# Kernel tuning notes

Measured on AMD Instinct MI355X. Metric: run time of the kernel, lower is better.

## Reference

```python
import jax, jax.numpy as jnp
import numpy as np

# Production-scale dims (see shape_source)
B, E, C = 4096, 512, 8            # batch, embeddingSize, dataChannels
N_UNITS, BASIS_K, MAX_DEPTH = 64, 16, 8
ENERGY_THR = 1e-3                  # routing.energyThr: stop when residual energy < thr * input energy
EPS = 1e-8


def setup_inputs() -> dict:
    key = jax.random.key(0)
    k1, k2, k3 = jax.random.split(key, 3)
    x = jax.random.normal(k1, (B, E, C), jnp.float32)
    # per-unit basis, columns L2-normalized along embedding dim (Unit basis vectors)
    basis = jax.random.normal(k2, (N_UNITS, E, BASIS_K), jnp.float32)
    basis = basis / (jnp.linalg.norm(basis, axis=1, keepdims=True) + EPS)
    # hash embedding = fixed random projection (generateHasher)
    hasher = jax.random.normal(k3, (E, E), jnp.float32) / np.sqrt(E)
    return {"x": x, "basis": basis, "hasher": hasher}


def reference(x, basis, hasher):
    """Hash-routed iterative matching pursuit.
    Each depth: hash-embed residual, score against all (non-masked) unit bases,
    pick best unit per sample, orthogonally project residual onto that unit's
    basis, subtract; stop (per-sample) when residual energy falls below threshold.
    Returns the accumulated reconstruction (network output).
    """
    init_energy = jnp.sum(x * x, axis=(1, 2))  # [B]
    unit_ids = jnp.arange(N_UNITS)

    def step(carry, _):
        r, out, used = carry  # r,out: [B,E,C]; used: [B,N] bool (lastCodes mask)
        # hash embedding of residual, normalized columns
        emb = jnp.einsum('ef,bfc->bec', hasher, r)
        emb = emb / (jnp.linalg.norm(emb, axis=1, keepdims=True) + EPS)
        # correlation of embedded residual with every unit basis vector
        corr = jnp.einsum('bec,nek->bnkc', emb, basis)       # [B,N,K,C]
        scores = jnp.sum(corr * corr, axis=(2, 3))            # [B,N]
        scores = jnp.where(used, -jnp.inf, scores)            # mask previously used units
        best = jnp.argmax(scores, axis=1)                     # [B] routing decision
        b_sel = basis[best]                                   # [B,E,K] gather selected unit basis
        # projection of raw residual onto selected basis
        coeffs = jnp.einsum('bec,bek->bkc', r, b_sel)         # [B,K,C]
        proj = jnp.einsum('bek,bkc->bec', b_sel, coeffs)      # [B,E,C]
        # per-sample stopping: residual energy vs threshold (depth pursuit)
        res_energy = jnp.sum(r * r, axis=(1, 2))              # [B]
        active = res_energy > ENERGY_THR * init_energy        # [B]
        a = active[:, None, None]
        out = out + jnp.where(a, proj, 0.0)
        r = jnp.where(a, r - proj, r)
        used = used | ((unit_ids[None, :] == best[:, None]) & active[:, None])
        return (r, out, used), None

    carry0 = (x, jnp.zeros_like(x), jnp.zeros((x.shape[0], N_UNITS), bool))
    (r, out, used), _ = jax.lax.scan(step, carry0, None, length=MAX_DEPTH)
    return out
```

## Files before the change

kernel.cpp:

```cpp
#include <hip/hip_runtime.h>
#include <math.h>

#define B_N 4096
#define E_N 512
#define C_N 8
#define NU 64
#define BK 16
#define NDEPTH 8
#define MROWS 1536
#define THR 0.001f
#define EPSV 1e-8f
#define NTOT (B_N * C_N)
#define WSCALE 64.0f
#define RSCALE 32.0f
#define RINV (1.0f / 32.0f)
#define FSP 520
#define BSP 17
#define CSP 516

typedef _Float16 f16;
typedef f16 f16x8 __attribute__((ext_vector_type(8)));
typedef float f32x4 __attribute__((ext_vector_type(4)));

__global__ void build_w(const float* __restrict__ basis,
                        const float* __restrict__ hasher,
                        f16* __restrict__ whi, f16* __restrict__ wlo) {
  const int m = blockIdx.x;
  const int t = threadIdx.x;
  float a0, a1;
  if (m < NU * BK) {
    const int n = m >> 4, k = m & 15;
    const float* bp = basis + (size_t)n * E_N * BK + k;
    a0 = 0.f; a1 = 0.f;
    for (int e = 0; e < E_N; ++e) {
      const float bv = bp[(size_t)e * BK];
      const float* hrow = hasher + (size_t)e * E_N;
      a0 = fmaf(bv, hrow[t], a0);
      a1 = fmaf(bv, hrow[t + 256], a1);
    }
  } else {
    const int e = m - NU * BK;
    a0 = hasher[(size_t)e * E_N + t];
    a1 = hasher[(size_t)e * E_N + t + 256];
  }
  a0 *= WSCALE; a1 *= WSCALE;
  const f16 h0 = (f16)a0, h1 = (f16)a1;
  whi[(size_t)m * E_N + t] = h0;
  wlo[(size_t)m * E_N + t] = (f16)(a0 - (float)h0);
  whi[(size_t)m * E_N + t + 256] = h1;
  wlo[(size_t)m * E_N + t + 256] = (f16)(a1 - (float)h1);
}

__launch_bounds__(256)
__global__ void init_convert(const float* __restrict__ x,
                             f16* __restrict__ rThi, f16* __restrict__ rTlo) {
  __shared__ float TT[C_N * FSP];
  const int tid = threadIdx.x;
  const int b = blockIdx.x;
  const float* xb = x + (size_t)b * E_N * C_N;
  for (int i = tid; i < E_N * C_N / 4; i += 256) {
    const float4 v = ((const float4*)xb)[i];
    const int e = i >> 1, c4 = (i & 1) * 4;
    TT[(c4 + 0) * FSP + e] = v.x;
    TT[(c4 + 1) * FSP + e] = v.y;
    TT[(c4 + 2) * FSP + e] = v.z;
    TT[(c4 + 3) * FSP + e] = v.w;
  }
  __syncthreads();
  const int c = tid >> 5, seg = tid & 31;
  const size_t row = ((size_t)b * C_N + c) * E_N;
#pragma unroll
  for (int hf = 0; hf < 2; ++hf) {
    const int e0 = seg * 16 + hf * 8;
    f16x8 oh, ol;
#pragma unroll
    for (int j = 0; j < 8; ++j) {
      const float v = TT[c * FSP + e0 + j] * RSCALE;
      const f16 h = (f16)v;
      oh[j] = h; ol[j] = (f16)(v - (float)h);
    }
    *(f16x8*)&rThi[row + e0] = oh;
    *(f16x8*)&rTlo[row + e0] = ol;
  }
}

__launch_bounds__(256, 2)
__global__ void mfma_score(const f16* __restrict__ whi, const f16* __restrict__ wlo,
                           const f16* __restrict__ rThi, const f16* __restrict__ rTlo,
                           float* __restrict__ part, float* __restrict__ nupart) {
  __shared__ f16 Ah[128 * 32], Al[128 * 32], Bh[128 * 32], Bl[128 * 32];
  __shared__ float nred[2][128];
  const int tid = threadIdx.x;
  const int lane = tid & 63;
  const int w = tid >> 6, wm = w >> 1, wn = w & 1;
  const int bid = blockIdx.x;
  const int nid = (bid & 7) * 384 + (bid >> 3);
  const int mt = nid % 12, nt = nid / 12;
  const int m0 = mt * 128;
  const int nq0 = nt * 128;
  const int l15 = lane & 15, lk = lane >> 4;
  const int rsw = lk ^ (l15 & 3) ^ ((l15 >> 2) & 3);

  const f32x4 fz = {0.f, 0.f, 0.f, 0.f};
  f32x4 acc[4][4];
#pragma unroll
  for (int i = 0; i < 4; ++i)
#pragma unroll
    for (int j = 0; j < 4; ++j) acc[i][j] = fz;

  const int h0 = tid, h1 = 256 + tid;
  const int r0 = h0 >> 2, c0 = h0 & 3, r1 = h1 >> 2, c1 = h1 & 3;
  const int s0 = (h0 & ~3) | (c0 ^ (r0 & 3) ^ ((r0 >> 2) & 3));
  const int s1 = (h1 & ~3) | (c1 ^ (r1 & 3) ^ ((r1 >> 2) & 3));
  const size_t aoff0 = (size_t)(m0 + r0) * E_N + c0 * 8;
  const size_t aoff1 = (size_t)(m0 + r1) * E_N + c1 * 8;
  const size_t boff0 = (size_t)(nq0 + r0) * E_N + c0 * 8;
  const size_t boff1 = (size_t)(nq0 + r1) * E_N + c1 * 8;

  f16x8 vah0 = *(const f16x8*)(whi + aoff0);
  f16x8 vah1 = *(const f16x8*)(whi + aoff1);
  f16x8 val0 = *(const f16x8*)(wlo + aoff0);
  f16x8 val1 = *(const f16x8*)(wlo + aoff1);
  f16x8 vbh0 = *(const f16x8*)(rThi + boff0);
  f16x8 vbh1 = *(const f16x8*)(rThi + boff1);
  f16x8 vbl0 = *(const f16x8*)(rTlo + boff0);
  f16x8 vbl1 = *(const f16x8*)(rTlo + boff1);

  for (int ks = 0; ks < 16; ++ks) {
    __syncthreads();
    ((f16x8*)Ah)[s0] = vah0; ((f16x8*)Ah)[s1] = vah1;
    ((f16x8*)Al)[s0] = val0; ((f16x8*)Al)[s1] = val1;
    ((f16x8*)Bh)[s0] = vbh0; ((f16x8*)Bh)[s1] = vbh1;
    ((f16x8*)Bl)[s0] = vbl0; ((f16x8*)Bl)[s1] = vbl1;
    __syncthreads();
    if (ks < 15) {
      const size_t ko = (size_t)(ks + 1) * 32;
      vah0 = *(const f16x8*)(whi + aoff0 + ko);
      vah1 = *(const f16x8*)(whi + aoff1 + ko);
      val0 = *(const f16x8*)(wlo + aoff0 + ko);
      val1 = *(const f16x8*)(wlo + aoff1 + ko);
      vbh0 = *(const f16x8*)(rThi + boff0 + ko);
      vbh1 = *(const f16x8*)(rThi + boff1 + ko);
      vbl0 = *(const f16x8*)(rTlo + boff0 + ko);
      vbl1 = *(const f16x8*)(rTlo + boff1 + ko);
    }
    f16x8 bhf[4], blf[4];
#pragma unroll
    for (int fn = 0; fn < 4; ++fn) {
      const int row = wn * 64 + fn * 16 + l15;
      const int idx = row * 4 + rsw;
      bhf[fn] = ((const f16x8*)Bh)[idx];
      blf[fn] = ((const f16x8*)Bl)[idx];
    }
#pragma unroll
    for (int fm = 0; fm < 4; ++fm) {
      const int row = wm * 64 + fm * 16 + l15;
      const int idx = row * 4 + rsw;
      const f16x8 ahf = ((const f16x8*)Ah)[idx];
      const f16x8 alf = ((const f16x8*)Al)[idx];
#pragma unroll
      for (int fn = 0; fn < 4; ++fn) {
        acc[fm][fn] = __builtin_amdgcn_mfma_f32_16x16x32_f16(ahf, bhf[fn], acc[fm][fn], 0, 0, 0);
        acc[fm][fn] = __builtin_amdgcn_mfma_f32_16x16x32_f16(ahf, blf[fn], acc[fm][fn], 0, 0, 0);
        acc[fm][fn] = __builtin_amdgcn_mfma_f32_16x16x32_f16(alf, bhf[fn], acc[fm][fn], 0, 0, 0);
      }
    }
  }

  if (m0 < NU * BK) {
#pragma unroll
    for (int fm = 0; fm < 4; ++fm) {
      const int u = (m0 >> 4) + wm * 4 + fm;
#pragma unroll
      for (int fn = 0; fn < 4; ++fn) {
        const f32x4 a = acc[fm][fn];
        float s = a.x * a.x + a.y * a.y + a.z * a.z + a.w * a.w;
        s += __shfl_xor(s, 16);
        s += __shfl_xor(s, 32);
        if (lk == 0)
          part[(size_t)u * NTOT + nq0 + wn * 64 + fn * 16 + l15] = s;
      }
    }
  } else {
#pragma unroll
    for (int fn = 0; fn < 4; ++fn) {
      float s = 0.f;
#pragma unroll
      for (int fm = 0; fm < 4; ++fm) {
        const f32x4 a = acc[fm][fn];
        s += a.x * a.x + a.y * a.y + a.z * a.z + a.w * a.w;
      }
      s += __shfl_xor(s, 16);
      s += __shfl_xor(s, 32);
      if (lk == 0) nred[wm][wn * 64 + fn * 16 + l15] = s;
    }
    __syncthreads();
    if (tid < 128)
      nupart[(size_t)((m0 - NU * BK) >> 7) * NTOT + nq0 + tid] =
          nred[0][tid] + nred[1][tid];
  }
}

__launch_bounds__(512, 2)
__global__ void apply_fused2(const float* __restrict__ basis,
                             f16* __restrict__ rThi, f16* __restrict__ rTlo,
                             const float* __restrict__ part,
                             const float* __restrict__ nupart,
                             unsigned char* __restrict__ used,
                             float* __restrict__ init_energy,
                             const int depth) {
  __shared__ float bsh[E_N * BSP];
  __shared__ float rsc[C_N * CSP];
  __shared__ float prt[4][BK * C_N];
  __shared__ float coeffs[BK * C_N];
  __shared__ float ew[8];
  __shared__ int sbu;
  __shared__ int act_sh;
  const int b = blockIdx.x;
  const int tid = threadIdx.x;
  const int c = tid >> 6, seg = tid & 63;
  const int e0 = seg * 8;
  const size_t row = ((size_t)b * C_N + c) * E_N;

  if (tid < NU) {
    float scale[C_N];
#pragma unroll
    for (int cc = 0; cc < C_N; ++cc) {
      float nu = 0.f;
#pragma unroll
      for (int t4 = 0; t4 < 4; ++t4)
        nu += nupart[(size_t)t4 * NTOT + b * C_N + cc];
      const float inv = 1.f / (sqrtf(nu) + EPSV);
      scale[cc] = inv * inv;
    }
    const float* pu = part + (size_t)tid * NTOT + b * C_N;
    float s = 0.f;
#pragma unroll
    for (int cc = 0; cc < C_N; ++cc) s = fmaf(pu[cc], scale[cc], s);
    if (used[(size_t)b * NU + tid]) s = -1.f;
    int idx = tid;
#pragma unroll
    for (int m = 1; m < 64; m <<= 1) {
      const float os = __shfl_xor(s, m);
      const int oi = __shfl_xor(idx, m);
      if (os > s || (os == s && oi < idx)) { s = os; idx = oi; }
    }
    if (tid == 0) sbu = idx;
  }
  float en = 0.f;
  {
    const f16x8 h = *(const f16x8*)&rThi[row + e0];
    const f16x8 l = *(const f16x8*)&rTlo[row + e0];
    float v4a[4], v4b[4];
#pragma unroll
    for (int j = 0; j < 4; ++j) {
      const float v = (float)h[j] + (float)l[j];
      v4a[j] = v; en = fmaf(v, v, en);
    }
#pragma unroll
    for (int j = 0; j < 4; ++j) {
      const float v = (float)h[4 + j] + (float)l[4 + j];
      v4b[j] = v; en = fmaf(v, v, en);
    }
    *(float4*)&rsc[c * CSP + e0]     = *(float4*)v4a;
    *(float4*)&rsc[c * CSP + e0 + 4] = *(float4*)v4b;
  }
  __syncthreads();

  const int bu = sbu;
  const float* bp = basis + (size_t)bu * E_N * BK;
  for (int i = tid; i < E_N * BK / 4; i += 512) {
    const float4 wv = ((const float4*)bp)[i];
    const int f0 = i * 4, e = f0 >> 4, k = f0 & 15;
    bsh[e * BSP + k] = wv.x;     bsh[e * BSP + k + 1] = wv.y;
    bsh[e * BSP + k + 2] = wv.z; bsh[e * BSP + k + 3] = wv.w;
  }
#pragma unroll
  for (int m = 1; m < 64; m <<= 1) en += __shfl_xor(en, m);
  if ((tid & 63) == 0) ew[tid >> 6] = en;
  __syncthreads();

  {
    const int k = tid >> 5, c2 = (tid >> 2) & 7, q = tid & 3;
    float s = 0.f;
    for (int i = 0; i < 128; ++i) {
      const int e = q + 4 * i;
      s = fmaf(bsh[e * BSP + k], rsc[c2 * CSP + e], s);
    }
    prt[q][k * C_N + c2] = s;
  }
  __syncthreads();

  if (tid < 128)
    coeffs[tid] = (prt[0][tid] + prt[1][tid]) + (prt[2][tid] + prt[3][tid]);
  if (tid == 128) {
    const float etot = ((ew[0] + ew[1]) + (ew[2] + ew[3])) +
                       ((ew[4] + ew[5]) + (ew[6] + ew[7]));
    float ie;
    if (depth == 0) { ie = etot; init_energy[b] = etot; }
    else ie = init_energy[b];
    act_sh = (etot > THR * ie) ? 1 : 0;
  }
  __syncthreads();

  if (act_sh) {
    const int e = tid;
    float bv[BK];
#pragma unroll
    for (int k = 0; k < BK; ++k) bv[k] = bsh[e * BSP + k];
#pragma unroll
    for (int cc = 0; cc < C_N; ++cc) {
      float pv = 0.f;
#pragma unroll
      for (int k = 0; k < BK; ++k) pv = fmaf(bv[k], coeffs[k * C_N + cc], pv);
      const float rv = rsc[cc * CSP + e] - pv;
      const f16 h = (f16)rv;
      rThi[((size_t)b * C_N + cc) * E_N + e] = h;
      rTlo[((size_t)b * C_N + cc) * E_N + e] = (f16)(rv - (float)h);
    }
    if (tid == 0) used[(size_t)b * NU + bu] = 1;
  }
}

__launch_bounds__(256)
__global__ void finalize2(const float* __restrict__ x,
                          const f16* __restrict__ rThi,
                          const f16* __restrict__ rTlo,
                          float* __restrict__ out) {
  __shared__ float TT[C_N * FSP];
  const int tid = threadIdx.x;
  const int b = blockIdx.x;
  const int c = tid >> 5, seg = tid & 31;
  const size_t row = ((size_t)b * C_N + c) * E_N;
#pragma unroll
  for (int hf = 0; hf < 2; ++hf) {
    const int e0 = seg * 16 + hf * 8;
    const f16x8 h = *(const f16x8*)&rThi[row + e0];
    const f16x8 l = *(const f16x8*)&rTlo[row + e0];
#pragma unroll
    for (int j = 0; j < 8; ++j)
      TT[c * FSP + e0 + j] = (float)h[j] + (float)l[j];
  }
  __syncthreads();
  const float* xb = x + (size_t)b * E_N * C_N;
  float* ob = out + (size_t)b * E_N * C_N;
  for (int i = tid; i < E_N * C_N / 4; i += 256) {
    const float4 xv = ((const float4*)xb)[i];
    const int e = i >> 1, c4 = (i & 1) * 4;
    float4 o;
    o.x = xv.x - TT[(c4 + 0) * FSP + e] * RINV;
    o.y = xv.y - TT[(c4 + 1) * FSP + e] * RINV;
    o.z = xv.z - TT[(c4 + 2) * FSP + e] * RINV;
    o.w = xv.w - TT[(c4 + 3) * FSP + e] * RINV;
    ((float4*)ob)[i] = o;
  }
}

extern "C" void kernel_launch(void* const* d_in, const int* in_sizes, int n_in,
                              void* d_out, int out_size, void* d_ws, size_t ws_size,
                              hipStream_t stream) {
  const float* x      = (const float*)d_in[0];
  const float* basis  = (const float*)d_in[1];
  const float* hasher = (const float*)d_in[2];
  float* out = (float*)d_out;

  float* part        = (float*)d_ws;
  float* nupart      = part + (size_t)NU * NTOT;
  float* init_energy = nupart + (size_t)4 * NTOT;
  f16*   whi         = (f16*)(init_energy + B_N);
  f16*   wlo         = whi + (size_t)MROWS * E_N;
  f16*   rThi        = wlo + (size_t)MROWS * E_N;
  f16*   rTlo        = rThi + (size_t)NTOT * E_N;
  unsigned char* used = (unsigned char*)(rTlo + (size_t)NTOT * E_N);

  hipMemsetAsync(used, 0, (size_t)B_N * NU, stream);
  build_w<<<MROWS, 256, 0, stream>>>(basis, hasher, whi, wlo);
  init_convert<<<B_N, 256, 0, stream>>>(x, rThi, rTlo);

  for (int d = 0; d < NDEPTH; ++d) {
    mfma_score<<<3072, 256, 0, stream>>>(whi, wlo, rThi, rTlo, part, nupart);
    apply_fused2<<<B_N, 512, 0, stream>>>(basis, rThi, rTlo, part, nupart,
                                          used, init_energy, d);
  }
  finalize2<<<B_N, 256, 0, stream>>>(x, rThi, rTlo, out);
}
```

Before: 1.768 ms.

## Track hashed-residual norms analytically instead of recomputing via GEMM each depth

The score GEMM used to compute both the unit correlations (1024 rows) and the full hashed-embedding norms (512 extra rows) on every depth. The norm is now computed once at depth 0 in a separate kernel. Afterwards it is updated in closed form from precomputed G=HᵀH products with each unit basis (GBs, BGB), which removes a third of the per-depth MFMA work. The cost is several setup kernels and extra per-sample reductions in the apply kernel. The fp32 recurrence may drift numerically from the directly recomputed norm and could flip argmax routing decisions.

```diff
diff --git a/kernel.cpp b/kernel.cpp
--- a/kernel.cpp
+++ b/kernel.cpp
@@ -84,19 +84,72 @@
   }
 }
 
+__global__ void ht_build(const float* __restrict__ hasher, float* __restrict__ HT) {
+  const int f = blockIdx.x;
+  for (int e = threadIdx.x; e < E_N; e += 256)
+    HT[(size_t)f * E_N + e] = hasher[(size_t)e * E_N + f];
+}
+
+__global__ void hb_build(const float* __restrict__ hasher,
+                         const float* __restrict__ basis, float* __restrict__ HBp) {
+  const int e = blockIdx.x;
+  const int t = threadIdx.x;
+  const int u = t >> 2, jg = (t & 3) * 4;
+  const float* hrow = hasher + (size_t)e * E_N;
+  float a0 = 0.f, a1 = 0.f, a2 = 0.f, a3 = 0.f;
+  for (int f = 0; f < E_N; ++f) {
+    const float h = hrow[f];
+    const float* bp = basis + ((size_t)u * E_N + f) * BK + jg;
+    a0 = fmaf(h, bp[0], a0); a1 = fmaf(h, bp[1], a1);
+    a2 = fmaf(h, bp[2], a2); a3 = fmaf(h, bp[3], a3);
+  }
+  float* o = HBp + ((size_t)u * E_N + e) * BK + jg;
+  o[0] = a0; o[1] = a1; o[2] = a2; o[3] = a3;
+}
+
+__global__ void gbs_build(const float* __restrict__ HT,
+                          const float* __restrict__ HBp, float* __restrict__ GBs) {
+  const int f = blockIdx.x;
+  const int t = threadIdx.x;
+  const int u = t >> 2, jg = (t & 3) * 4;
+  const float* hrow = HT + (size_t)f * E_N;
+  float a0 = 0.f, a1 = 0.f, a2 = 0.f, a3 = 0.f;
+  for (int e = 0; e < E_N; ++e) {
+    const float h = hrow[e];
+    const float* bp = HBp + ((size_t)u * E_N + e) * BK + jg;
+    a0 = fmaf(h, bp[0], a0); a1 = fmaf(h, bp[1], a1);
+    a2 = fmaf(h, bp[2], a2); a3 = fmaf(h, bp[3], a3);
+  }
+  const float s = WSCALE * WSCALE;
+  float* o = GBs + ((size_t)u * E_N + f) * BK + jg;
+  o[0] = a0 * s; o[1] = a1 * s; o[2] = a2 * s; o[3] = a3 * s;
+}
+
+__global__ void bgb_build(const float* __restrict__ basis,
+                          const float* __restrict__ GBs, float* __restrict__ BGB) {
+  const int u = blockIdx.x;
+  const int t = threadIdx.x;
+  const int j = t >> 4, j2 = t & 15;
+  float a = 0.f;
+  for (int e = 0; e < E_N; ++e)
+    a = fmaf(basis[((size_t)u * E_N + e) * BK + j],
+             GBs[((size_t)u * E_N + e) * BK + j2], a);
+  BGB[(size_t)u * 256 + t] = a;
+}
+
 __launch_bounds__(256, 2)
-__global__ void mfma_score(const f16* __restrict__ whi, const f16* __restrict__ wlo,
-                           const f16* __restrict__ rThi, const f16* __restrict__ rTlo,
-                           float* __restrict__ part, float* __restrict__ nupart) {
+__global__ void init_norm(const f16* __restrict__ whi, const f16* __restrict__ wlo,
+                          const f16* __restrict__ rThi, const f16* __restrict__ rTlo,
+                          float* __restrict__ nupart) {
   __shared__ f16 Ah[128 * 32], Al[128 * 32], Bh[128 * 32], Bl[128 * 32];
   __shared__ float nred[2][128];
   const int tid = threadIdx.x;
   const int lane = tid & 63;
   const int w = tid >> 6, wm = w >> 1, wn = w & 1;
   const int bid = blockIdx.x;
-  const int nid = (bid & 7) * 384 + (bid >> 3);
-  const int mt = nid % 12, nt = nid / 12;
-  const int m0 = mt * 128;
+  const int nid = (bid & 7) * 128 + (bid >> 3);
+  const int mt = nid % 4, nt = nid / 4;
+  const int m0 = NU * BK + mt * 128;
   const int nq0 = nt * 128;
   const int l15 = lane & 15, lk = lane >> 4;
   const int rsw = lk ^ (l15 & 3) ^ ((l15 >> 2) & 3);
@@ -166,46 +219,127 @@
       }
     }
   }
-
-  if (m0 < NU * BK) {
+#pragma unroll
+  for (int fn = 0; fn < 4; ++fn) {
+    float s = 0.f;
 #pragma unroll
     for (int fm = 0; fm < 4; ++fm) {
-      const int u = (m0 >> 4) + wm * 4 + fm;
+      const f32x4 a = acc[fm][fn];
+      s += a.x * a.x + a.y * a.y + a.z * a.z + a.w * a.w;
+    }
+    s += __shfl_xor(s, 16);
+    s += __shfl_xor(s, 32);
+    if (lk == 0) nred[wm][wn * 64 + fn * 16 + l15] = s;
+  }
+  __syncthreads();
+  if (tid < 128)
+    nupart[(size_t)mt * NTOT + nq0 + tid] = nred[0][tid] + nred[1][tid];
+}
+
+__launch_bounds__(256, 2)
+__global__ void mfma_score(const f16* __restrict__ whi, const f16* __restrict__ wlo,
+                           const f16* __restrict__ rThi, const f16* __restrict__ rTlo,
+                           float* __restrict__ part) {
+  __shared__ f16 Ah[128 * 32], Al[128 * 32], Bh[128 * 32], Bl[128 * 32];
+  const int tid = threadIdx.x;
+  const int lane = tid & 63;
+  const int w = tid >> 6, wm = w >> 1, wn = w & 1;
+  const int bid = blockIdx.x;
+  const int nid = (bid & 7) * 256 + (bid >> 3);
+  const int mt = nid % 8, nt = nid / 8;
+  const int m0 = mt * 128;
+  const int nq0 = nt * 128;
+  const int l15 = lane & 15, lk = lane >> 4;
+  const int rsw = lk ^ (l15 & 3) ^ ((l15 >> 2) & 3);
+
+  const f32x4 fz = {0.f, 0.f, 0.f, 0.f};
+  f32x4 acc[4][4];
+#pragma unroll
+  for (int i = 0; i < 4; ++i)
+#pragma unroll
+    for (int j = 0; j < 4; ++j) acc[i][j] = fz;
+
+  const int h0 = tid, h1 = 256 + tid;
+  const int r0 = h0 >> 2, c0 = h0 & 3, r1 = h1 >> 2, c1 = h1 & 3;
+  const int s0 = (h0 & ~3) | (c0 ^ (r0 & 3) ^ ((r0 >> 2) & 3));
+  const int s1 = (h1 & ~3) | (c1 ^ (r1 & 3) ^ ((r1 >> 2) & 3));
+  const size_t aoff0 = (size_t)(m0 + r0) * E_N + c0 * 8;
+  const size_t aoff1 = (size_t)(m0 + r1) * E_N + c1 * 8;
+  const size_t boff0 = (size_t)(nq0 + r0) * E_N + c0 * 8;
+  const size_t boff1 = (size_t)(nq0 + r1) * E_N + c1 * 8;
+
+  f16x8 vah0 = *(const f16x8*)(whi + aoff0);
+  f16x8 vah1 = *(const f16x8*)(whi + aoff1);
+  f16x8 val0 = *(const f16x8*)(wlo + aoff0);
+  f16x8 val1 = *(const f16x8*)(wlo + aoff1);
+  f16x8 vbh0 = *(const f16x8*)(rThi + boff0);
+  f16x8 vbh1 = *(const f16x8*)(rThi + boff1);
+  f16x8 vbl0 = *(const f16x8*)(rTlo + boff0);
+  f16x8 vbl1 = *(const f16x8*)(rTlo + boff1);
+
+  for (int ks = 0; ks < 16; ++ks) {
+    __syncthreads();
+    ((f16x8*)Ah)[s0] = vah0; ((f16x8*)Ah)[s1] = vah1;
+    ((f16x8*)Al)[s0] = val0; ((f16x8*)Al)[s1] = val1;
+    ((f16x8*)Bh)[s0] = vbh0; ((f16x8*)Bh)[s1] = vbh1;
+    ((f16x8*)Bl)[s0] = vbl0; ((f16x8*)Bl)[s1] = vbl1;
+    __syncthreads();
+    if (ks < 15) {
+      const size_t ko = (size_t)(ks + 1) * 32;
+      vah0 = *(const f16x8*)(whi + aoff0 + ko);
+      vah1 = *(const f16x8*)(whi + aoff1 + ko);
+      val0 = *(const f16x8*)(wlo + aoff0 + ko);
+      val1 = *(const f16x8*)(wlo + aoff1 + ko);
+      vbh0 = *(const f16x8*)(rThi + boff0 + ko);
+      vbh1 = *(const f16x8*)(rThi + boff1 + ko);
+      vbl0 = *(const f16x8*)(rTlo + boff0 + ko);
+      vbl1 = *(const f16x8*)(rTlo + boff1 + ko);
+    }
+    f16x8 bhf[4], blf[4];
+#pragma unroll
+    for (int fn = 0; fn < 4; ++fn) {
+      const int row = wn * 64 + fn * 16 + l15;
+      const int idx = row * 4 + rsw;
+      bhf[fn] = ((const f16x8*)Bh)[idx];
+      blf[fn] = ((const f16x8*)Bl)[idx];
+    }
+#pragma unroll
+    for (int fm = 0; fm < 4; ++fm) {
+      const int row = wm * 64 + fm * 16 + l15;
+      const int idx = row * 4 + rsw;
+      const f16x8 ahf = ((const f16x8*)Ah)[idx];
+      const f16x8 alf = ((const f16x8*)Al)[idx];
 #pragma unroll
       for (int fn = 0; fn < 4; ++fn) {
-        const f32x4 a = acc[fm][fn];
-        float s = a.x * a.x + a.y * a.y + a.z * a.z + a.w * a.w;
-        s += __shfl_xor(s, 16);
-        s += __shfl_xor(s, 32);
-        if (lk == 0)
-          part[(size_t)u * NTOT + nq0 + wn * 64 + fn * 16 + l15] = s;
+        acc[fm][fn] = __builtin_amdgcn_mfma_f32_16x16x32_f16(ahf, bhf[fn], acc[fm][fn], 0, 0, 0);
+        acc[fm][fn] = __builtin_amdgcn_mfma_f32_16x16x32_f16(ahf, blf[fn], acc[fm][fn], 0, 0, 0);
+        acc[fm][fn] = __builtin_amdgcn_mfma_f32_16x16x32_f16(alf, bhf[fn], acc[fm][fn], 0, 0, 0);
       }
     }
-  } else {
+  }
+#pragma unroll
+  for (int fm = 0; fm < 4; ++fm) {
+    const int u = (m0 >> 4) + wm * 4 + fm;
 #pragma unroll
     for (int fn = 0; fn < 4; ++fn) {
-      float s = 0.f;
-#pragma unroll
-      for (int fm = 0; fm < 4; ++fm) {
-        const f32x4 a = acc[fm][fn];
-        s += a.x * a.x + a.y * a.y + a.z * a.z + a.w * a.w;
-      }
+      const f32x4 a = acc[fm][fn];
+      float s = a.x * a.x + a.y * a.y + a.z * a.z + a.w * a.w;
       s += __shfl_xor(s, 16);
       s += __shfl_xor(s, 32);
-      if (lk == 0) nred[wm][wn * 64 + fn * 16 + l15] = s;
-    }
-    __syncthreads();
-    if (tid < 128)
-      nupart[(size_t)((m0 - NU * BK) >> 7) * NTOT + nq0 + tid] =
-          nred[0][tid] + nred[1][tid];
+      if (lk == 0)
+        part[(size_t)u * NTOT + nq0 + wn * 64 + fn * 16 + l15] = s;
+    }
   }
 }
 
 __launch_bounds__(512, 2)
-__global__ void apply_fused2(const float* __restrict__ basis,
+__global__ void apply_fused3(const float* __restrict__ basis,
                              f16* __restrict__ rThi, f16* __restrict__ rTlo,
                              const float* __restrict__ part,
                              const float* __restrict__ nupart,
+                             float* __restrict__ nu,
+                             const float* __restrict__ GBs,
+                             const float* __restrict__ BGB,
                              unsigned char* __restrict__ used,
                              float* __restrict__ init_energy,
                              const int depth) {
@@ -226,11 +360,16 @@
     float scale[C_N];
 #pragma unroll
     for (int cc = 0; cc < C_N; ++cc) {
-      float nu = 0.f;
-#pragma unroll
-      for (int t4 = 0; t4 < 4; ++t4)
-        nu += nupart[(size_t)t4 * NTOT + b * C_N + cc];
-      const float inv = 1.f / (sqrtf(nu) + EPSV);
+      float nuv;
+      if (depth == 0) {
+        nuv = 0.f;
+#pragma unroll
+        for (int t4 = 0; t4 < 4; ++t4)
+          nuv += nupart[(size_t)t4 * NTOT + b * C_N + cc];
+      } else {
+        nuv = nu[(size_t)b * C_N + cc];
+      }
+      const float inv = 1.f / (sqrtf(nuv) + EPSV);
       scale[cc] = inv * inv;
     }
     const float* pu = part + (size_t)tid * NTOT + b * C_N;
@@ -319,6 +458,46 @@
       rTlo[((size_t)b * C_N + cc) * E_N + e] = (f16)(rv - (float)h);
     }
     if (tid == 0) used[(size_t)b * NU + bu] = 1;
+  }
+
+  {
+    const int j = tid >> 5, c2 = (tid >> 2) & 7, q = tid & 3;
+    const float* gbp = GBs + (size_t)bu * E_N * BK;
+    float s = 0.f;
+    for (int i = 0; i < 128; ++i) {
+      const int e = q + 4 * i;
+      s = fmaf(gbp[(size_t)e * BK + j], rsc[c2 * CSP + e], s);
+    }
+    prt[q][j * C_N + c2] = s;
+  }
+  __syncthreads();
+
+  if (tid < C_N) {
+    const int cc = tid;
+    float A = 0.f, Bt = 0.f;
+    const float* bgb = BGB + (size_t)bu * 256;
+#pragma unroll
+    for (int j = 0; j < BK; ++j) {
+      const float cross = (prt[0][j * C_N + cc] + prt[1][j * C_N + cc]) +
+                          (prt[2][j * C_N + cc] + prt[3][j * C_N + cc]);
+      const float cj = coeffs[j * C_N + cc];
+      A = fmaf(cj, cross, A);
+      float tmp = 0.f;
+#pragma unroll
+      for (int j2 = 0; j2 < BK; ++j2)
+        tmp = fmaf(bgb[j * BK + j2], coeffs[j2 * C_N + cc], tmp);
+      Bt = fmaf(cj, tmp, Bt);
+    }
+    float nu_base;
+    if (depth == 0) {
+      nu_base = 0.f;
+#pragma unroll
+      for (int t4 = 0; t4 < 4; ++t4)
+        nu_base += nupart[(size_t)t4 * NTOT + b * C_N + cc];
+    } else {
+      nu_base = nu[(size_t)b * C_N + cc];
+    }
+    nu[(size_t)b * C_N + cc] = act_sh ? (nu_base - 2.f * A + Bt) : nu_base;
   }
 }
 
@@ -366,8 +545,13 @@
 
   float* part        = (float*)d_ws;
   float* nupart      = part + (size_t)NU * NTOT;
-  float* init_energy = nupart + (size_t)4 * NTOT;
-  f16*   whi         = (f16*)(init_energy + B_N);
+  float* nu          = nupart + (size_t)4 * NTOT;
+  float* init_energy = nu + (size_t)NTOT;
+  float* HT          = init_energy + B_N;
+  float* HBp         = HT + (size_t)E_N * E_N;
+  float* GBs         = HBp + (size_t)NU * E_N * BK;
+  float* BGB         = GBs + (size_t)NU * E_N * BK;
+  f16*   whi         = (f16*)(BGB + (size_t)NU * 256);
   f16*   wlo         = whi + (size_t)MROWS * E_N;
   f16*   rThi        = wlo + (size_t)MROWS * E_N;
   f16*   rTlo        = rThi + (size_t)NTOT * E_N;
@@ -376,11 +560,16 @@
   hipMemsetAsync(used, 0, (size_t)B_N * NU, stream);
   build_w<<<MROWS, 256, 0, stream>>>(basis, hasher, whi, wlo);
   init_convert<<<B_N, 256, 0, stream>>>(x, rThi, rTlo);
+  ht_build<<<E_N, 256, 0, stream>>>(hasher, HT);
+  hb_build<<<E_N, 256, 0, stream>>>(hasher, basis, HBp);
+  gbs_build<<<E_N, 256, 0, stream>>>(HT, HBp, GBs);
+  bgb_build<<<NU, 256, 0, stream>>>(basis, GBs, BGB);
+  init_norm<<<1024, 256, 0, stream>>>(whi, wlo, rThi, rTlo, nupart);
 
   for (int d = 0; d < NDEPTH; ++d) {
-    mfma_score<<<3072, 256, 0, stream>>>(whi, wlo, rThi, rTlo, part, nupart);
-    apply_fused2<<<B_N, 512, 0, stream>>>(basis, rThi, rTlo, part, nupart,
-                                          used, init_energy, d);
+    mfma_score<<<2048, 256, 0, stream>>>(whi, wlo, rThi, rTlo, part);
+    apply_fused3<<<B_N, 512, 0, stream>>>(basis, rThi, rTlo, part, nupart,
+                                          nu, GBs, BGB, used, init_energy, d);
   }
   finalize2<<<B_N, 256, 0, stream>>>(x, rThi, rTlo, out);
 }
```

After: 2.439 ms. 1.38x slower.
